# Performance work log

Measured on AMD Instinct MI355X. Metric: run time of the kernel, lower is better.

The kernel has to match this reference:

```python
import jax, jax.numpy as jnp
import numpy as np

B, S, HID = 2, 2048, 2048
H, D, KV = 16, 128, 4          # heads, head_dim, kv heads
REP = H // KV                  # GQA repeat factor
THETA = 10000.0


def setup_inputs() -> dict:
    key = jax.random.key(0)
    ks = jax.random.split(key, 12)
    query = jax.random.normal(ks[0], (B, S, HID), jnp.float32)
    k_in = jax.random.normal(ks[1], (B, S, HID), jnp.float32)
    v_in = jax.random.normal(ks[2], (B, S, HID), jnp.float32)
    # additive causal mask: 0 on/below diag, -10000 above
    causal = jnp.tril(jnp.ones((S, S), jnp.float32))
    mask = jnp.broadcast_to((1.0 - causal) * -10000.0, (B, 1, S, S))
    # rotary tables (cos/sin of freqs_cis), shape [S, D//2]
    inv_freq = 1.0 / (THETA ** (jnp.arange(0, D, 2, dtype=jnp.float32) / D))
    ang = jnp.outer(jnp.arange(S, dtype=jnp.float32), inv_freq)
    freqs_cos, freqs_sin = jnp.cos(ang), jnp.sin(ang)
    sd = 0.02
    Wq = jax.random.normal(ks[3], (HID, H * D), jnp.float32) * sd
    bq = jnp.zeros((H * D,), jnp.float32)
    Wk = jax.random.normal(ks[4], (HID, KV * D), jnp.float32) * sd
    bk = jnp.zeros((KV * D,), jnp.float32)
    Wv = jax.random.normal(ks[5], (HID, KV * D), jnp.float32) * sd
    bv = jnp.zeros((KV * D,), jnp.float32)
    Wo = jax.random.normal(ks[6], (H * D, HID), jnp.float32) * sd
    bo = jnp.zeros((HID,), jnp.float32)
    return {"query": query, "key": k_in, "value": v_in, "mask": mask,
            "freqs_cos": freqs_cos, "freqs_sin": freqs_sin,
            "Wq": Wq, "bq": bq, "Wk": Wk, "bk": bk,
            "Wv": Wv, "bv": bv, "Wo": Wo, "bo": bo}


def _rope(x, cos, sin):
    # x: [B,S,h,D]; pairs adjacent dims as complex (view_as_complex)
    xr = x.reshape(*x.shape[:-1], D // 2, 2)
    xe, xo = xr[..., 0], xr[..., 1]
    c = cos[None, :, None, :]
    s = sin[None, :, None, :]
    re = xe * c - xo * s
    im = xe * s + xo * c
    return jnp.stack([re, im], axis=-1).reshape(x.shape)


def reference(query, key, value, mask, freqs_cos, freqs_sin,
              Wq, bq, Wk, bk, Wv, bv, Wo, bo):
    q = (query @ Wq + bq).reshape(B, S, H, D)
    k = (key @ Wk + bk).reshape(B, S, KV, D)
    v = (value @ Wv + bv).reshape(B, S, KV, D)
    # repeat_kv: torch.repeat_interleave along head dim
    k = jnp.repeat(k, REP, axis=2)
    v = jnpp_repeat = jnp.repeat(v, REP, axis=2)
    q = _rope(q, freqs_cos, freqs_sin)
    k = _rope(k, freqs_cos, freqs_sin)
    q = q.transpose(0, 2, 1, 3)  # [B,H,S,D]
    k = k.transpose(0, 2, 1, 3)
    v = v.transpose(0, 2, 1, 3)
    scores = jnp.einsum('bhqd,bhkd->bhqk', q, k) / jnp.sqrt(jnp.float32(D))
    scores = scores + mask
    probs = jax.nn.softmax(scores, axis=-1)
    ctx = jnp.einsum('bhqk,bhkd->bhqd', probs, v)
    ctx = ctx.transpose(0, 2, 1, 3).reshape(B, S, H * D)
    return ctx @ Wo + bo
```

## Files before the change

kernel.cpp:

```cpp
#include <hip/hip_runtime.h>
#include <stdint.h>

#define BB 2
#define SS 2048
#define HID 2048
#define NH 16
#define DD 128
#define NKV 4

typedef unsigned short u16;
typedef __attribute__((ext_vector_type(8))) short short8;
typedef __attribute__((ext_vector_type(4))) float f32x4;

#if __has_builtin(__builtin_amdgcn_exp2f)
#define EXP2(x) __builtin_amdgcn_exp2f(x)
#else
#define EXP2(x) exp2f(x)
#endif

__device__ __forceinline__ u16 f2bf(float x) {
    union { float f; unsigned u; } v; v.f = x;
    unsigned u = v.u;
    return (u16)((u + 0x7FFFu + ((u >> 16) & 1u)) >> 16);
}

__device__ __forceinline__ void async_lds16(const void* g, void* l) {
    __builtin_amdgcn_global_load_lds(
        (const __attribute__((address_space(1))) void*)(uintptr_t)g,
        (__attribute__((address_space(3))) void*)(uintptr_t)l,
        16, 0, 0);
}

__global__ __launch_bounds__(256) void k_prep(const float* __restrict__ query,
                                              const float* __restrict__ key,
                                              const float* __restrict__ value,
                                              const float* __restrict__ Wq,
                                              const float* __restrict__ Wk,
                                              const float* __restrict__ Wv,
                                              const float* __restrict__ Wo,
                                              u16* __restrict__ qbf,
                                              u16* __restrict__ kbf,
                                              u16* __restrict__ vbf,
                                              u16* __restrict__ Wt,
                                              u16* __restrict__ Wot) {
    __shared__ float tile[32][33];
    int x = blockIdx.x;
    if (x < 24576) {
        const float* in; u16* out;
        if (x < 8192)       { in = query; out = qbf; }
        else if (x < 16384) { in = key;   out = kbf; x -= 8192; }
        else                { in = value; out = vbf; x -= 16384; }
        const int i = x * 256 + threadIdx.x;
        float4 v = ((const float4*)in)[i];
        uint2 o;
        o.x = (unsigned)f2bf(v.x) | ((unsigned)f2bf(v.y) << 16);
        o.y = (unsigned)f2bf(v.z) | ((unsigned)f2bf(v.w) << 16);
        ((uint2*)out)[i] = o;
        return;
    }
    const int v_ = x - 24576;
    const int ty = v_ / 160;
    const int xt = v_ - ty * 160;
    const float* src; u16* dst; int N, n0;
    if (xt < 64)      { src = Wq; dst = Wt;                          N = 2048; n0 = xt * 32; }
    else if (xt < 80) { src = Wk; dst = Wt + (size_t)2048 * 2048;    N = 512;  n0 = (xt - 64) * 32; }
    else if (xt < 96) { src = Wv; dst = Wt + (size_t)2560 * 2048;    N = 512;  n0 = (xt - 80) * 32; }
    else              { src = Wo; dst = Wot;                         N = 2048; n0 = (xt - 96) * 32; }
    const int k0 = ty * 32;
    const int c = threadIdx.x & 31, r = threadIdx.x >> 5;
#pragma unroll
    for (int i = 0; i < 32; i += 8)
        tile[r + i][c] = src[(size_t)(k0 + r + i) * N + n0 + c];
    __syncthreads();
#pragma unroll
    for (int i = 0; i < 32; i += 8)
        dst[(size_t)(n0 + r + i) * 2048 + k0 + c] = f2bf(tile[c][r + i]);
}

__global__ __launch_bounds__(256) void k_gemm_qkv(const u16* __restrict__ qbf,
                                                  const u16* __restrict__ kbf,
                                                  const u16* __restrict__ vbf,
                                                  const u16* __restrict__ Wt,
                                                  const float* __restrict__ bq,
                                                  const float* __restrict__ bk,
                                                  const float* __restrict__ bv,
                                                  const float* __restrict__ fc,
                                                  const float* __restrict__ fs,
                                                  u16* __restrict__ qro,
                                                  u16* __restrict__ kro,
                                                  u16* __restrict__ vtr) {
    __shared__ char smem[32768];
    u16* As = (u16*)smem;
    u16* Bs = (u16*)(smem + 16384);
    float* Ep = (float*)smem;

    const int tid = threadIdx.x;
    const int lane = tid & 63, wave = tid >> 6;
    const int bn = blockIdx.x;
    const int bm = blockIdx.y * 128;
    const u16* A = (bn < 16) ? qbf : (bn < 20) ? kbf : vbf;

    const int srow = wave * 8 + (lane >> 3);
    const int c0 = ((lane & 7) ^ (lane >> 3)) * 8;
    const u16* gA = A  + (size_t)(bm + srow) * 2048 + c0;
    const u16* gB = Wt + (size_t)(bn * 128 + srow) * 2048 + c0;

    const int r = lane & 15, q4 = lane >> 4;
    const int wm = (wave & 1) * 64, wn = (wave >> 1) * 64;

    int aoff[4][2], boff[4][2];
#pragma unroll
    for (int i = 0; i < 4; i++) {
        const int ar = wm + i * 16 + r;
        const int pa = q4 ^ (ar & 7);
        aoff[i][0] = ar * 64 + pa * 8;
        aoff[i][1] = ar * 64 + (pa ^ 4) * 8;
        const int br = wn + i * 16 + r;
        const int pb = q4 ^ (br & 7);
        boff[i][0] = br * 64 + pb * 8;
        boff[i][1] = br * 64 + (pb ^ 4) * 8;
    }

    f32x4 acc[4][4] = {};

    for (int kb = 0; kb < 2048; kb += 64) {
        async_lds16(gA,                       As + wave * 512);
        async_lds16(gA + (size_t)32 * 2048,   As + 2048 + wave * 512);
        async_lds16(gA + (size_t)64 * 2048,   As + 4096 + wave * 512);
        async_lds16(gA + (size_t)96 * 2048,   As + 6144 + wave * 512);
        async_lds16(gB,                       Bs + wave * 512);
        async_lds16(gB + (size_t)32 * 2048,   Bs + 2048 + wave * 512);
        async_lds16(gB + (size_t)64 * 2048,   Bs + 4096 + wave * 512);
        async_lds16(gB + (size_t)96 * 2048,   Bs + 6144 + wave * 512);
        gA += 64; gB += 64;
        __syncthreads();

#pragma unroll
        for (int kk = 0; kk < 2; kk++) {
            short8 av[4], bv_[4];
#pragma unroll
            for (int i = 0; i < 4; i++) av[i] = *(const short8*)(As + aoff[i][kk]);
#pragma unroll
            for (int j = 0; j < 4; j++) bv_[j] = *(const short8*)(Bs + boff[j][kk]);
#pragma unroll
            for (int i = 0; i < 4; i++)
#pragma unroll
                for (int j = 0; j < 4; j++)
                    acc[i][j] = __builtin_amdgcn_mfma_f32_16x16x32_bf16(av[i], bv_[j], acc[i][j], 0, 0, 0);
        }
        __syncthreads();
    }

    if (bn < 20) {
        const bool isQ = (bn < 16);
        const float qsc = isQ ? 0.08838834764831845f * 1.4426950408889634f : 1.0f;
        const float* bias = isQ ? bq : bk;
        const int head = isQ ? bn : (bn - 16);
        u16* base = isQ ? qro : kro;
        const int nheads = isQ ? NH : NKV;

        float* ep = Ep + wave * 1280;
        const int rowg = bm + wm + lane;
        const int s = rowg & 2047, bidx = rowg >> 11;
        const float* fcp0 = fc + s * 64;
        const float* fsp0 = fs + s * 64;

#pragma unroll
        for (int j = 0; j < 4; j++) {
            const float bcol = bias[head * 128 + wn + j * 16 + r];
#pragma unroll
            for (int i = 0; i < 4; i++)
#pragma unroll
                for (int g = 0; g < 4; g++)
                    ep[(i * 16 + q4 * 4 + g) * 20 + r] = acc[i][j][g] + bcol;
            float4 x0 = *(float4*)(ep + lane * 20 + 0);
            float4 x1 = *(float4*)(ep + lane * 20 + 4);
            float4 x2 = *(float4*)(ep + lane * 20 + 8);
            float4 x3 = *(float4*)(ep + lane * 20 + 12);
            const int d0 = wn + j * 16;
            const int ii0 = d0 >> 1;
            float4 ca = *(const float4*)(fcp0 + ii0);
            float4 cb = *(const float4*)(fcp0 + ii0 + 4);
            float4 sa = *(const float4*)(fsp0 + ii0);
            float4 sb = *(const float4*)(fsp0 + ii0 + 4);
            float o[16];
            o[0]  = (x0.x * ca.x - x0.y * sa.x) * qsc;  o[1]  = (x0.x * sa.x + x0.y * ca.x) * qsc;
            o[2]  = (x0.z * ca.y - x0.w * sa.y) * qsc;  o[3]  = (x0.z * sa.y + x0.w * ca.y) * qsc;
            o[4]  = (x1.x * ca.z - x1.y * sa.z) * qsc;  o[5]  = (x1.x * sa.z + x1.y * ca.z) * qsc;
            o[6]  = (x1.z * ca.w - x1.w * sa.w) * qsc;  o[7]  = (x1.z * sa.w + x1.w * ca.w) * qsc;
            o[8]  = (x2.x * cb.x - x2.y * sb.x) * qsc;  o[9]  = (x2.x * sb.x + x2.y * cb.x) * qsc;
            o[10] = (x2.z * cb.y - x2.w * sb.y) * qsc;  o[11] = (x2.z * sb.y + x2.w * cb.y) * qsc;
            o[12] = (x3.x * cb.z - x3.y * sb.z) * qsc;  o[13] = (x3.x * sb.z + x3.y * cb.z) * qsc;
            o[14] = (x3.z * cb.w - x3.w * sb.w) * qsc;  o[15] = (x3.z * sb.w + x3.w * cb.w) * qsc;
            unsigned w0 = (unsigned)f2bf(o[0])  | ((unsigned)f2bf(o[1])  << 16);
            unsigned w1 = (unsigned)f2bf(o[2])  | ((unsigned)f2bf(o[3])  << 16);
            unsigned w2 = (unsigned)f2bf(o[4])  | ((unsigned)f2bf(o[5])  << 16);
            unsigned w3 = (unsigned)f2bf(o[6])  | ((unsigned)f2bf(o[7])  << 16);
            unsigned w4 = (unsigned)f2bf(o[8])  | ((unsigned)f2bf(o[9])  << 16);
            unsigned w5 = (unsigned)f2bf(o[10]) | ((unsigned)f2bf(o[11]) << 16);
            unsigned w6 = (unsigned)f2bf(o[12]) | ((unsigned)f2bf(o[13]) << 16);
            unsigned w7 = (unsigned)f2bf(o[14]) | ((unsigned)f2bf(o[15]) << 16);
            u16* dst = base + (((size_t)(bidx * nheads + head) * SS + s) << 7) + d0;
            *(uint4*)dst = make_uint4(w0, w1, w2, w3);
            *(uint4*)(dst + 8) = make_uint4(w4, w5, w6, w7);
        }
    } else {
#pragma unroll
        for (int j = 0; j < 4; j++) {
            const int col = bn * 128 + wn + j * 16 + r - 2560;
            const int d = col & 127, kv = col >> 7;
            const float bb = bv[col];
#pragma unroll
            for (int i = 0; i < 4; i++) {
                const int row0 = bm + wm + i * 16 + q4 * 4;
                const int s0 = row0 & 2047, b = row0 >> 11;
                uint2 o;
                o.x = (unsigned)f2bf(acc[i][j][0] + bb) | ((unsigned)f2bf(acc[i][j][1] + bb) << 16);
                o.y = (unsigned)f2bf(acc[i][j][2] + bb) | ((unsigned)f2bf(acc[i][j][3] + bb) << 16);
                *(uint2*)(vtr + ((size_t)(b * NKV + kv) * DD + d) * SS + s0) = o;
            }
        }
    }
}

__global__ __launch_bounds__(256) void k_gemm_bt(const u16* __restrict__ A,
                                                 const u16* __restrict__ Bt,
                                                 const float* __restrict__ bias,
                                                 float* __restrict__ C,
                                                 int M, int N, int K) {
    __shared__ char smem[32768];
    u16* As = (u16*)smem;
    u16* Bs = (u16*)(smem + 16384);

    const int tid = threadIdx.x;
    const int lane = tid & 63, wave = tid >> 6;
    const int bm = blockIdx.y * 128, bn = blockIdx.x * 128;

    const int srow = wave * 8 + (lane >> 3);
    const int c0 = ((lane & 7) ^ (lane >> 3)) * 8;
    const u16* gA = A  + (size_t)(bm + srow) * K + c0;
    const u16* gB = Bt + (size_t)(bn + srow) * K + c0;

    const int r = lane & 15, q4 = lane >> 4;
    const int wm = (wave & 1) * 64, wn = (wave >> 1) * 64;

    int aoff[4][2], boff[4][2];
#pragma unroll
    for (int i = 0; i < 4; i++) {
        const int ar = wm + i * 16 + r;
        const int pa = q4 ^ (ar & 7);
        aoff[i][0] = ar * 64 + pa * 8;
        aoff[i][1] = ar * 64 + (pa ^ 4) * 8;
        const int br = wn + i * 16 + r;
        const int pb = q4 ^ (br & 7);
        boff[i][0] = br * 64 + pb * 8;
        boff[i][1] = br * 64 + (pb ^ 4) * 8;
    }

    f32x4 acc[4][4] = {};

    for (int kb = 0; kb < K; kb += 64) {
        async_lds16(gA,                    As + wave * 512);
        async_lds16(gA + (size_t)32 * K,   As + 2048 + wave * 512);
        async_lds16(gA + (size_t)64 * K,   As + 4096 + wave * 512);
        async_lds16(gA + (size_t)96 * K,   As + 6144 + wave * 512);
        async_lds16(gB,                    Bs + wave * 512);
        async_lds16(gB + (size_t)32 * K,   Bs + 2048 + wave * 512);
        async_lds16(gB + (size_t)64 * K,   Bs + 4096 + wave * 512);
        async_lds16(gB + (size_t)96 * K,   Bs + 6144 + wave * 512);
        gA += 64; gB += 64;
        __syncthreads();

#pragma unroll
        for (int kk = 0; kk < 2; kk++) {
            short8 av[4], bv_[4];
#pragma unroll
            for (int i = 0; i < 4; i++) av[i] = *(const short8*)(As + aoff[i][kk]);
#pragma unroll
            for (int j = 0; j < 4; j++) bv_[j] = *(const short8*)(Bs + boff[j][kk]);
#pragma unroll
            for (int i = 0; i < 4; i++)
#pragma unroll
                for (int j = 0; j < 4; j++)
                    acc[i][j] = __builtin_amdgcn_mfma_f32_16x16x32_bf16(av[i], bv_[j], acc[i][j], 0, 0, 0);
        }
        __syncthreads();
    }

#pragma unroll
    for (int j = 0; j < 4; j++) {
        const int col = bn + wn + j * 16 + r;
        const float bb = bias[col];
#pragma unroll
        for (int i = 0; i < 4; i++) {
            const int row = bm + wm + i * 16 + q4 * 4;
#pragma unroll
            for (int g = 0; g < 4; g++)
                C[(size_t)(row + g) * N + col] = acc[i][j][g] + bb;
        }
    }
}

__global__ __launch_bounds__(256) void k_attn(const u16* __restrict__ Q,
                                              const u16* __restrict__ K_,
                                              const u16* __restrict__ V_,
                                              u16* __restrict__ Ctx) {
    __shared__ u16 Ks[32 * 128];
    __shared__ u16 Vs[128 * 32];
    __shared__ u16 Pb[4 * 32 * 40];

    const int tid = threadIdx.x;
    const int lane = tid & 63, wave = tid >> 6;
    const int bh = blockIdx.x;
    const int b = bh >> 4, h = bh & 15;
    const int kvh = (b << 2) | (h >> 2);
    const int qb = (gridDim.y - 1 - blockIdx.y) * 128;
    const int qcol = lane & 15, q4 = lane >> 4;
    const int qw = qb + wave * 32;

    const u16* Qg = Q + ((size_t)bh * SS + qw + qcol) * DD;
    short8 qfr[2][4];
#pragma unroll
    for (int qi = 0; qi < 2; qi++)
#pragma unroll
        for (int c = 0; c < 4; c++)
            qfr[qi][c] = *(const short8*)(Qg + qi * 16 * DD + c * 32 + q4 * 8);

    const u16* Kg = K_ + (size_t)kvh * SS * DD;
    const u16* Vg = V_ + (size_t)kvh * DD * SS;

    const int krow = tid >> 4;
    const int kchunk = (tid & 15) ^ (krow & 7);
    const int vd = tid >> 2;
    const int vchunk = (tid & 3) ^ ((vd >> 1) & 3);

    f32x4 lacc[2] = {};
    f32x4 oacc[2][8] = {};

    const short8 ones = {0x3F80, 0x3F80, 0x3F80, 0x3F80, 0x3F80, 0x3F80, 0x3F80, 0x3F80};
    u16* pb = Pb + wave * 1280;
    unsigned* pb32 = (unsigned*)pb;

    for (int kb = 0; kb < qb + 128; kb += 32) {
        async_lds16(Kg + (size_t)(kb + krow) * DD + kchunk * 8,       Ks + wave * 512);
        async_lds16(Kg + (size_t)(kb + 16 + krow) * DD + kchunk * 8,  Ks + 2048 + wave * 512);
        async_lds16(Vg + (size_t)vd * SS + kb + vchunk * 8,           Vs + wave * 512);
        async_lds16(Vg + (size_t)(vd + 64) * SS + kb + vchunk * 8,    Vs + 2048 + wave * 512);
        __syncthreads();

        if (kb <= qw + 31) {
            f32x4 sc[2][2] = {};
#pragma unroll
            for (int kt = 0; kt < 2; kt++) {
                const int kr = kt * 16 + qcol;
#pragma unroll
                for (int c = 0; c < 4; c++) {
                    short8 kf = *(const short8*)(Ks + kr * 128 + (((c * 4 + q4) ^ (kr & 7)) << 3));
                    sc[kt][0] = __builtin_amdgcn_mfma_f32_16x16x32_bf16(kf, qfr[0][c], sc[kt][0], 0, 0, 0);
                    sc[kt][1] = __builtin_amdgcn_mfma_f32_16x16x32_bf16(kf, qfr[1][c], sc[kt][1], 0, 0, 0);
                }
            }

            if (kb + 32 > qw) {
#pragma unroll
                for (int kt = 0; kt < 2; kt++)
#pragma unroll
                    for (int qi = 0; qi < 2; qi++)
#pragma unroll
                        for (int g = 0; g < 4; g++) {
                            const int key = kb + kt * 16 + q4 * 4 + g;
                            if (key > qw + qi * 16 + qcol) sc[kt][qi][g] = -1e30f;
                        }
            }

            const unsigned sel = 0x07060302u;
#pragma unroll
            for (int qi = 0; qi < 2; qi++) {
                float p0 = EXP2(sc[0][qi][0]), p1 = EXP2(sc[0][qi][1]);
                float p2 = EXP2(sc[0][qi][2]), p3 = EXP2(sc[0][qi][3]);
                float p4 = EXP2(sc[1][qi][0]), p5 = EXP2(sc[1][qi][1]);
                float p6 = EXP2(sc[1][qi][2]), p7 = EXP2(sc[1][qi][3]);
                unsigned pk0 = __builtin_amdgcn_perm(__float_as_uint(p1), __float_as_uint(p0), sel);
                unsigned pk1 = __builtin_amdgcn_perm(__float_as_uint(p3), __float_as_uint(p2), sel);
                unsigned pk2 = __builtin_amdgcn_perm(__float_as_uint(p5), __float_as_uint(p4), sel);
                unsigned pk3 = __builtin_amdgcn_perm(__float_as_uint(p7), __float_as_uint(p6), sel);
                const int row = qi * 16 + qcol;
                *(uint2*)(pb32 + row * 20 + 2 * q4)     = make_uint2(pk0, pk1);
                *(uint2*)(pb32 + row * 20 + 8 + 2 * q4) = make_uint2(pk2, pk3);
            }

            short8 pf0 = *(const short8*)(pb + qcol * 40 + q4 * 8);
            short8 pf1 = *(const short8*)(pb + (16 + qcol) * 40 + q4 * 8);

            lacc[0] = __builtin_amdgcn_mfma_f32_16x16x32_bf16(ones, pf0, lacc[0], 0, 0, 0);
            lacc[1] = __builtin_amdgcn_mfma_f32_16x16x32_bf16(ones, pf1, lacc[1], 0, 0, 0);
#pragma unroll
            for (int dt = 0; dt < 8; dt++) {
                const int vr = dt * 16 + qcol;
                short8 vfr = *(const short8*)(Vs + vr * 32 + ((q4 ^ ((vr >> 1) & 3)) << 3));
                oacc[0][dt] = __builtin_amdgcn_mfma_f32_16x16x32_bf16(vfr, pf0, oacc[0][dt], 0, 0, 0);
                oacc[1][dt] = __builtin_amdgcn_mfma_f32_16x16x32_bf16(vfr, pf1, oacc[1][dt], 0, 0, 0);
            }
        }
        __syncthreads();
    }

#pragma unroll
    for (int qi = 0; qi < 2; qi++) {
        const float inv = 1.0f / lacc[qi][0];
        u16* outp = Ctx + ((size_t)b * SS + qw + qi * 16 + qcol) * (NH * DD) + h * DD;
#pragma unroll
        for (int dt = 0; dt < 8; dt++) {
            unsigned lo = (unsigned)f2bf(oacc[qi][dt][0] * inv) | ((unsigned)f2bf(oacc[qi][dt][1] * inv) << 16);
            unsigned hi = (unsigned)f2bf(oacc[qi][dt][2] * inv) | ((unsigned)f2bf(oacc[qi][dt][3] * inv) << 16);
            *(uint2*)(outp + dt * 16 + q4 * 4) = make_uint2(lo, hi);
        }
    }
}

extern "C" void kernel_launch(void* const* d_in, const int* in_sizes, int n_in,
                              void* d_out, int out_size, void* d_ws, size_t ws_size,
                              hipStream_t stream) {
    const float* query = (const float*)d_in[0];
    const float* key   = (const float*)d_in[1];
    const float* value = (const float*)d_in[2];
    const float* fc    = (const float*)d_in[4];
    const float* fs    = (const float*)d_in[5];
    const float* Wq    = (const float*)d_in[6];
    const float* bq    = (const float*)d_in[7];
    const float* Wk    = (const float*)d_in[8];
    const float* bk    = (const float*)d_in[9];
    const float* Wv    = (const float*)d_in[10];
    const float* bv    = (const float*)d_in[11];
    const float* Wo    = (const float*)d_in[12];
    const float* bo    = (const float*)d_in[13];
    float* out = (float*)d_out;

    char* w = (char*)d_ws;
    u16* qbf = (u16*)(w);
    u16* kbf = (u16*)(w + 16777216);
    u16* vbf = (u16*)(w + 33554432);
    u16* Wt  = (u16*)(w + 50331648);
    u16* Wot = (u16*)(w + 62914560);
    u16* qro = (u16*)(w + 71303168);
    u16* kro = (u16*)(w + 88080384);
    u16* vtr = (u16*)(w + 92274688);
    u16* ctx = (u16*)(w + 96468992);

    k_prep<<<34816, 256, 0, stream>>>(query, key, value, Wq, Wk, Wv, Wo,
                                      qbf, kbf, vbf, Wt, Wot);
    k_gemm_qkv<<<dim3(24, 32), 256, 0, stream>>>(qbf, kbf, vbf, Wt, bq, bk, bv,
                                                 fc, fs, qro, kro, vtr);
    k_attn<<<dim3(32, 16), 256, 0, stream>>>(qro, kro, vtr, ctx);
    k_gemm_bt<<<dim3(16, 32), 256, 0, stream>>>(ctx, Wot, bo, out, 4096, 2048, 2048);
}
```

Baseline: 400.5 us.

## Use 256x256 double-buffered pipelined GEMM tiles with 8 waves for projections

Replaces the 128x128 single-buffered GEMM loop in both the QKV projection and output projection with a shared 256x256-tile routine. It uses 512 threads, 128KB of LDS, double buffering, staggered async prefetch of A and B tiles interleaved with MFMA phases, and s_setprio around the compute. The goal is to hide global load latency and raise reuse per tile. The trade-off is far fewer blocks (192 and 128), which can under-fill the 256 CUs, plus heavy LDS use and register pressure.

```diff
diff --git a/kernel.cpp b/kernel.cpp
--- a/kernel.cpp
+++ b/kernel.cpp
@@ -77,142 +77,228 @@
         dst[(size_t)(n0 + r + i) * 2048 + k0 + c] = f2bf(tile[c][r + i]);
 }
 
-__global__ __launch_bounds__(256) void k_gemm_qkv(const u16* __restrict__ qbf,
-                                                  const u16* __restrict__ kbf,
-                                                  const u16* __restrict__ vbf,
-                                                  const u16* __restrict__ Wt,
-                                                  const float* __restrict__ bq,
-                                                  const float* __restrict__ bk,
-                                                  const float* __restrict__ bv,
-                                                  const float* __restrict__ fc,
-                                                  const float* __restrict__ fs,
-                                                  u16* __restrict__ qro,
-                                                  u16* __restrict__ kro,
-                                                  u16* __restrict__ vtr) {
-    __shared__ char smem[32768];
+__device__ __forceinline__ void gemm256_loop(const u16* __restrict__ gA,
+                                             const u16* __restrict__ gB,
+                                             const int K, char* smem,
+                                             const int wave, const int lane,
+                                             f32x4 (&acc)[8][4]) {
+    const int r = lane & 15, q4 = lane >> 4;
+    const int wr = wave >> 2, wc = wave & 3;
     u16* As = (u16*)smem;
-    u16* Bs = (u16*)(smem + 16384);
-    float* Ep = (float*)smem;
-
+    u16* Bs = (u16*)(smem + 65536);
+
+    int aoff[8], boff[4];
+#pragma unroll
+    for (int i = 0; i < 8; i++) {
+        const int ar = wr * 128 + i * 16 + r;
+        aoff[i] = ar * 64 + ((q4 ^ (ar & 7)) << 3);
+    }
+#pragma unroll
+    for (int j = 0; j < 4; j++) {
+        const int br = wc * 64 + j * 16 + r;
+        boff[j] = br * 64 + ((q4 ^ (br & 7)) << 3);
+    }
+
+    const int nt = K >> 6;
+
+#define STG_A(buf, i, T) async_lds16(gA + (size_t)(i) * 64 * K + (size_t)(T) * 64, \
+                                     smem + (buf) * 32768 + ((i) * 64 + wave * 8) * 128)
+#define STG_B(buf, i, T) async_lds16(gB + (size_t)(i) * 64 * K + (size_t)(T) * 64, \
+                                     smem + 65536 + (buf) * 32768 + ((i) * 64 + wave * 8) * 128)
+
+    STG_A(0, 0, 0); STG_A(0, 1, 0); STG_A(0, 2, 0); STG_A(0, 3, 0);
+    STG_B(0, 0, 0); STG_B(0, 1, 0); STG_B(0, 2, 0); STG_B(0, 3, 0);
+    STG_B(1, 0, 1); STG_B(1, 1, 1); STG_B(1, 2, 1); STG_B(1, 3, 1);
+    asm volatile("s_waitcnt vmcnt(4)" ::: "memory");
+    __builtin_amdgcn_s_barrier();
+
+    short8 Af[4][2], Bf[4][2];
+    for (int t = 0; t < nt; t++) {
+        const int cur = t & 1;
+        const u16* Ab = As + cur * 16384;
+        const u16* Bb = Bs + cur * 16384;
+        const bool p1v = (t + 1 < nt);
+        const bool p2v = (t + 2 < nt);
+
+#pragma unroll
+        for (int i = 0; i < 4; i++) {
+            Af[i][0] = *(const short8*)(Ab + aoff[i]);
+            Af[i][1] = *(const short8*)(Ab + (aoff[i] ^ 32));
+        }
+#pragma unroll
+        for (int j = 0; j < 2; j++) {
+            Bf[j][0] = *(const short8*)(Bb + boff[j]);
+            Bf[j][1] = *(const short8*)(Bb + (boff[j] ^ 32));
+        }
+        if (p1v) { STG_A(cur ^ 1, 0, t + 1); STG_A(cur ^ 1, 1, t + 1); }
+        __builtin_amdgcn_s_barrier();
+        asm volatile("s_waitcnt lgkmcnt(0)" ::: "memory");
+        __builtin_amdgcn_s_setprio(1);
+#pragma unroll
+        for (int kk = 0; kk < 2; kk++)
+#pragma unroll
+            for (int i = 0; i < 4; i++)
+#pragma unroll
+                for (int j = 0; j < 2; j++)
+                    acc[i][j] = __builtin_amdgcn_mfma_f32_16x16x32_bf16(Af[i][kk], Bf[j][kk], acc[i][j], 0, 0, 0);
+        __builtin_amdgcn_s_setprio(0);
+        __builtin_amdgcn_s_barrier();
+
+#pragma unroll
+        for (int j = 2; j < 4; j++) {
+            Bf[j][0] = *(const short8*)(Bb + boff[j]);
+            Bf[j][1] = *(const short8*)(Bb + (boff[j] ^ 32));
+        }
+        if (p1v) { STG_A(cur ^ 1, 2, t + 1); STG_A(cur ^ 1, 3, t + 1); }
+        __builtin_amdgcn_s_barrier();
+        asm volatile("s_waitcnt lgkmcnt(0)" ::: "memory");
+        __builtin_amdgcn_s_setprio(1);
+#pragma unroll
+        for (int kk = 0; kk < 2; kk++)
+#pragma unroll
+            for (int i = 0; i < 4; i++)
+#pragma unroll
+                for (int j = 2; j < 4; j++)
+                    acc[i][j] = __builtin_amdgcn_mfma_f32_16x16x32_bf16(Af[i][kk], Bf[j][kk], acc[i][j], 0, 0, 0);
+        __builtin_amdgcn_s_setprio(0);
+        __builtin_amdgcn_s_barrier();
+
+#pragma unroll
+        for (int i = 0; i < 4; i++) {
+            Af[i][0] = *(const short8*)(Ab + aoff[i + 4]);
+            Af[i][1] = *(const short8*)(Ab + (aoff[i + 4] ^ 32));
+        }
+        if (p2v) { STG_B(cur, 0, t + 2); STG_B(cur, 1, t + 2); }
+        __builtin_amdgcn_s_barrier();
+        asm volatile("s_waitcnt lgkmcnt(0)" ::: "memory");
+        __builtin_amdgcn_s_setprio(1);
+#pragma unroll
+        for (int kk = 0; kk < 2; kk++)
+#pragma unroll
+            for (int i = 0; i < 4; i++)
+#pragma unroll
+                for (int j = 2; j < 4; j++)
+                    acc[i + 4][j] = __builtin_amdgcn_mfma_f32_16x16x32_bf16(Af[i][kk], Bf[j][kk], acc[i + 4][j], 0, 0, 0);
+        __builtin_amdgcn_s_setprio(0);
+        __builtin_amdgcn_s_barrier();
+
+        if (p2v) {
+            STG_B(cur, 2, t + 2); STG_B(cur, 3, t + 2);
+            asm volatile("s_waitcnt vmcnt(4)" ::: "memory");
+        } else {
+            asm volatile("s_waitcnt vmcnt(0)" ::: "memory");
+        }
+        __builtin_amdgcn_s_barrier();
+        __builtin_amdgcn_s_setprio(1);
+#pragma unroll
+        for (int kk = 0; kk < 2; kk++)
+#pragma unroll
+            for (int i = 0; i < 4; i++)
+#pragma unroll
+                for (int j = 0; j < 2; j++)
+                    acc[i + 4][j] = __builtin_amdgcn_mfma_f32_16x16x32_bf16(Af[i][kk], Bf[j][kk], acc[i + 4][j], 0, 0, 0);
+        __builtin_amdgcn_s_setprio(0);
+        __builtin_amdgcn_s_barrier();
+    }
+#undef STG_A
+#undef STG_B
+}
+
+__global__ __launch_bounds__(512, 2) void k_gemm_qkv(const u16* __restrict__ qbf,
+                                                     const u16* __restrict__ kbf,
+                                                     const u16* __restrict__ vbf,
+                                                     const u16* __restrict__ Wt,
+                                                     const float* __restrict__ bq,
+                                                     const float* __restrict__ bk,
+                                                     const float* __restrict__ bv,
+                                                     const float* __restrict__ fc,
+                                                     const float* __restrict__ fs,
+                                                     u16* __restrict__ qro,
+                                                     u16* __restrict__ kro,
+                                                     u16* __restrict__ vtr) {
+    __shared__ char smem[131072];
     const int tid = threadIdx.x;
     const int lane = tid & 63, wave = tid >> 6;
-    const int bn = blockIdx.x;
-    const int bm = blockIdx.y * 128;
-    const u16* A = (bn < 16) ? qbf : (bn < 20) ? kbf : vbf;
+    const int wr = wave >> 2, wc = wave & 3;
+    const int r = lane & 15, q4 = lane >> 4;
+    const int bx = blockIdx.x;
+    const int bm0 = blockIdx.y * 256;
+    const u16* A = (bx < 8) ? qbf : (bx < 10) ? kbf : vbf;
 
     const int srow = wave * 8 + (lane >> 3);
     const int c0 = ((lane & 7) ^ (lane >> 3)) * 8;
-    const u16* gA = A  + (size_t)(bm + srow) * 2048 + c0;
-    const u16* gB = Wt + (size_t)(bn * 128 + srow) * 2048 + c0;
-
-    const int r = lane & 15, q4 = lane >> 4;
-    const int wm = (wave & 1) * 64, wn = (wave >> 1) * 64;
-
-    int aoff[4][2], boff[4][2];
-#pragma unroll
-    for (int i = 0; i < 4; i++) {
-        const int ar = wm + i * 16 + r;
-        const int pa = q4 ^ (ar & 7);
-        aoff[i][0] = ar * 64 + pa * 8;
-        aoff[i][1] = ar * 64 + (pa ^ 4) * 8;
-        const int br = wn + i * 16 + r;
-        const int pb = q4 ^ (br & 7);
-        boff[i][0] = br * 64 + pb * 8;
-        boff[i][1] = br * 64 + (pb ^ 4) * 8;
-    }
-
-    f32x4 acc[4][4] = {};
-
-    for (int kb = 0; kb < 2048; kb += 64) {
-        async_lds16(gA,                       As + wave * 512);
-        async_lds16(gA + (size_t)32 * 2048,   As + 2048 + wave * 512);
-        async_lds16(gA + (size_t)64 * 2048,   As + 4096 + wave * 512);
-        async_lds16(gA + (size_t)96 * 2048,   As + 6144 + wave * 512);
-        async_lds16(gB,                       Bs + wave * 512);
-        async_lds16(gB + (size_t)32 * 2048,   Bs + 2048 + wave * 512);
-        async_lds16(gB + (size_t)64 * 2048,   Bs + 4096 + wave * 512);
-        async_lds16(gB + (size_t)96 * 2048,   Bs + 6144 + wave * 512);
-        gA += 64; gB += 64;
-        __syncthreads();
-
-#pragma unroll
-        for (int kk = 0; kk < 2; kk++) {
-            short8 av[4], bv_[4];
-#pragma unroll
-            for (int i = 0; i < 4; i++) av[i] = *(const short8*)(As + aoff[i][kk]);
-#pragma unroll
-            for (int j = 0; j < 4; j++) bv_[j] = *(const short8*)(Bs + boff[j][kk]);
-#pragma unroll
-            for (int i = 0; i < 4; i++)
-#pragma unroll
-                for (int j = 0; j < 4; j++)
-                    acc[i][j] = __builtin_amdgcn_mfma_f32_16x16x32_bf16(av[i], bv_[j], acc[i][j], 0, 0, 0);
-        }
-        __syncthreads();
-    }
-
-    if (bn < 20) {
-        const bool isQ = (bn < 16);
+    const u16* gA = A  + (size_t)(bm0 + srow) * 2048 + c0;
+    const u16* gB = Wt + (size_t)(bx * 256 + srow) * 2048 + c0;
+
+    f32x4 acc[8][4] = {};
+    gemm256_loop(gA, gB, 2048, smem, wave, lane, acc);
+
+    if (bx < 10) {
+        const bool isQ = (bx < 8);
         const float qsc = isQ ? 0.08838834764831845f * 1.4426950408889634f : 1.0f;
         const float* bias = isQ ? bq : bk;
-        const int head = isQ ? bn : (bn - 16);
         u16* base = isQ ? qro : kro;
         const int nheads = isQ ? NH : NKV;
 
-        float* ep = Ep + wave * 1280;
-        const int rowg = bm + wm + lane;
-        const int s = rowg & 2047, bidx = rowg >> 11;
-        const float* fcp0 = fc + s * 64;
-        const float* fsp0 = fs + s * 64;
-
+        float* ep = (float*)smem + wave * 2560;
 #pragma unroll
         for (int j = 0; j < 4; j++) {
-            const float bcol = bias[head * 128 + wn + j * 16 + r];
-#pragma unroll
-            for (int i = 0; i < 4; i++)
+            const int gc = bx * 256 + wc * 64 + j * 16;
+            const int head = isQ ? (gc >> 7) : ((gc - 2048) >> 7);
+            const int d0 = gc & 127;
+            const float bcol = bias[head * 128 + d0 + r];
+#pragma unroll
+            for (int i = 0; i < 8; i++)
 #pragma unroll
                 for (int g = 0; g < 4; g++)
                     ep[(i * 16 + q4 * 4 + g) * 20 + r] = acc[i][j][g] + bcol;
-            float4 x0 = *(float4*)(ep + lane * 20 + 0);
-            float4 x1 = *(float4*)(ep + lane * 20 + 4);
-            float4 x2 = *(float4*)(ep + lane * 20 + 8);
-            float4 x3 = *(float4*)(ep + lane * 20 + 12);
-            const int d0 = wn + j * 16;
-            const int ii0 = d0 >> 1;
-            float4 ca = *(const float4*)(fcp0 + ii0);
-            float4 cb = *(const float4*)(fcp0 + ii0 + 4);
-            float4 sa = *(const float4*)(fsp0 + ii0);
-            float4 sb = *(const float4*)(fsp0 + ii0 + 4);
-            float o[16];
-            o[0]  = (x0.x * ca.x - x0.y * sa.x) * qsc;  o[1]  = (x0.x * sa.x + x0.y * ca.x) * qsc;
-            o[2]  = (x0.z * ca.y - x0.w * sa.y) * qsc;  o[3]  = (x0.z * sa.y + x0.w * ca.y) * qsc;
-            o[4]  = (x1.x * ca.z - x1.y * sa.z) * qsc;  o[5]  = (x1.x * sa.z + x1.y * ca.z) * qsc;
-            o[6]  = (x1.z * ca.w - x1.w * sa.w) * qsc;  o[7]  = (x1.z * sa.w + x1.w * ca.w) * qsc;
-            o[8]  = (x2.x * cb.x - x2.y * sb.x) * qsc;  o[9]  = (x2.x * sb.x + x2.y * cb.x) * qsc;
-            o[10] = (x2.z * cb.y - x2.w * sb.y) * qsc;  o[11] = (x2.z * sb.y + x2.w * cb.y) * qsc;
-            o[12] = (x3.x * cb.z - x3.y * sb.z) * qsc;  o[13] = (x3.x * sb.z + x3.y * cb.z) * qsc;
-            o[14] = (x3.z * cb.w - x3.w * sb.w) * qsc;  o[15] = (x3.z * sb.w + x3.w * cb.w) * qsc;
-            unsigned w0 = (unsigned)f2bf(o[0])  | ((unsigned)f2bf(o[1])  << 16);
-            unsigned w1 = (unsigned)f2bf(o[2])  | ((unsigned)f2bf(o[3])  << 16);
-            unsigned w2 = (unsigned)f2bf(o[4])  | ((unsigned)f2bf(o[5])  << 16);
-            unsigned w3 = (unsigned)f2bf(o[6])  | ((unsigned)f2bf(o[7])  << 16);
-            unsigned w4 = (unsigned)f2bf(o[8])  | ((unsigned)f2bf(o[9])  << 16);
-            unsigned w5 = (unsigned)f2bf(o[10]) | ((unsigned)f2bf(o[11]) << 16);
-            unsigned w6 = (unsigned)f2bf(o[12]) | ((unsigned)f2bf(o[13]) << 16);
-            unsigned w7 = (unsigned)f2bf(o[14]) | ((unsigned)f2bf(o[15]) << 16);
-            u16* dst = base + (((size_t)(bidx * nheads + head) * SS + s) << 7) + d0;
-            *(uint4*)dst = make_uint4(w0, w1, w2, w3);
-            *(uint4*)(dst + 8) = make_uint4(w4, w5, w6, w7);
+#pragma unroll
+            for (int rr = 0; rr < 2; rr++) {
+                const int row = rr * 64 + lane;
+                const int grow = bm0 + wr * 128 + row;
+                const int s = grow & 2047, bidx = grow >> 11;
+                const float* fcp0 = fc + s * 64;
+                const float* fsp0 = fs + s * 64;
+                float4 x0 = *(float4*)(ep + row * 20 + 0);
+                float4 x1 = *(float4*)(ep + row * 20 + 4);
+                float4 x2 = *(float4*)(ep + row * 20 + 8);
+                float4 x3 = *(float4*)(ep + row * 20 + 12);
+                const int ii0 = d0 >> 1;
+                float4 ca = *(const float4*)(fcp0 + ii0);
+                float4 cb = *(const float4*)(fcp0 + ii0 + 4);
+                float4 sa = *(const float4*)(fsp0 + ii0);
+                float4 sb = *(const float4*)(fsp0 + ii0 + 4);
+                float o[16];
+                o[0]  = (x0.x * ca.x - x0.y * sa.x) * qsc;  o[1]  = (x0.x * sa.x + x0.y * ca.x) * qsc;
+                o[2]  = (x0.z * ca.y - x0.w * sa.y) * qsc;  o[3]  = (x0.z * sa.y + x0.w * ca.y) * qsc;
+                o[4]  = (x1.x * ca.z - x1.y * sa.z) * qsc;  o[5]  = (x1.x * sa.z + x1.y * ca.z) * qsc;
+                o[6]  = (x1.z * ca.w - x1.w * sa.w) * qsc;  o[7]  = (x1.z * sa.w + x1.w * ca.w) * qsc;
+                o[8]  = (x2.x * cb.x - x2.y * sb.x) * qsc;  o[9]  = (x2.x * sb.x + x2.y * cb.x) * qsc;
+                o[10] = (x2.z * cb.y - x2.w * sb.y) * qsc;  o[11] = (x2.z * sb.y + x2.w * cb.y) * qsc;
+                o[12] = (x3.x * cb.z - x3.y * sb.z) * qsc;  o[13] = (x3.x * sb.z + x3.y * cb.z) * qsc;
+                o[14] = (x3.z * cb.w - x3.w * sb.w) * qsc;  o[15] = (x3.z * sb.w + x3.w * cb.w) * qsc;
+                unsigned w0 = (unsigned)f2bf(o[0])  | ((unsigned)f2bf(o[1])  << 16);
+                unsigned w1 = (unsigned)f2bf(o[2])  | ((unsigned)f2bf(o[3])  << 16);
+                unsigned w2 = (unsigned)f2bf(o[4])  | ((unsigned)f2bf(o[5])  << 16);
+                unsigned w3 = (unsigned)f2bf(o[6])  | ((unsigned)f2bf(o[7])  << 16);
+                unsigned w4 = (unsigned)f2bf(o[8])  | ((unsigned)f2bf(o[9])  << 16);
+                unsigned w5 = (unsigned)f2bf(o[10]) | ((unsigned)f2bf(o[11]) << 16);
+                unsigned w6 = (unsigned)f2bf(o[12]) | ((unsigned)f2bf(o[13]) << 16);
+                unsigned w7 = (unsigned)f2bf(o[14]) | ((unsigned)f2bf(o[15]) << 16);
+                u16* dst = base + (((size_t)(bidx * nheads + head) * SS + s) << 7) + d0;
+                *(uint4*)dst = make_uint4(w0, w1, w2, w3);
+                *(uint4*)(dst + 8) = make_uint4(w4, w5, w6, w7);
+            }
         }
     } else {
 #pragma unroll
         for (int j = 0; j < 4; j++) {
-            const int col = bn * 128 + wn + j * 16 + r - 2560;
-            const int d = col & 127, kv = col >> 7;
-            const float bb = bv[col];
-#pragma unroll
-            for (int i = 0; i < 4; i++) {
-                const int row0 = bm + wm + i * 16 + q4 * 4;
+            const int colb = bx * 256 + wc * 64 + j * 16 + r - 2560;
+            const int d = colb & 127, kv = colb >> 7;
+            const float bb = bv[colb];
+#pragma unroll
+            for (int i = 0; i < 8; i++) {
+                const int row0 = bm0 + wr * 128 + i * 16 + q4 * 4;
                 const int s0 = row0 & 2047, b = row0 >> 11;
                 uint2 o;
                 o.x = (unsigned)f2bf(acc[i][j][0] + bb) | ((unsigned)f2bf(acc[i][j][1] + bb) << 16);
@@ -223,77 +309,33 @@
     }
 }
 
-__global__ __launch_bounds__(256) void k_gemm_bt(const u16* __restrict__ A,
-                                                 const u16* __restrict__ Bt,
-                                                 const float* __restrict__ bias,
-                                                 float* __restrict__ C,
-                                                 int M, int N, int K) {
-    __shared__ char smem[32768];
-    u16* As = (u16*)smem;
-    u16* Bs = (u16*)(smem + 16384);
-
+__global__ __launch_bounds__(512, 2) void k_gemm_bt(const u16* __restrict__ A,
+                                                    const u16* __restrict__ Bt,
+                                                    const float* __restrict__ bias,
+                                                    float* __restrict__ C,
+                                                    int M, int N, int K) {
+    __shared__ char smem[131072];
     const int tid = threadIdx.x;
     const int lane = tid & 63, wave = tid >> 6;
-    const int bm = blockIdx.y * 128, bn = blockIdx.x * 128;
+    const int wr = wave >> 2, wc = wave & 3;
+    const int r = lane & 15, q4 = lane >> 4;
+    const int bm0 = blockIdx.y * 256, bn0 = blockIdx.x * 256;
 
     const int srow = wave * 8 + (lane >> 3);
     const int c0 = ((lane & 7) ^ (lane >> 3)) * 8;
-    const u16* gA = A  + (size_t)(bm + srow) * K + c0;
-    const u16* gB = Bt + (size_t)(bn + srow) * K + c0;
-
-    const int r = lane & 15, q4 = lane >> 4;
-    const int wm = (wave & 1) * 64, wn = (wave >> 1) * 64;
-
-    int aoff[4][2], boff[4][2];
-#pragma unroll
-    for (int i = 0; i < 4; i++) {
-        const int ar = wm + i * 16 + r;
-        const int pa = q4 ^ (ar & 7);
-        aoff[i][0] = ar * 64 + pa * 8;
-        aoff[i][1] = ar * 64 + (pa ^ 4) * 8;
-        const int br = wn + i * 16 + r;
-        const int pb = q4 ^ (br & 7);
-        boff[i][0] = br * 64 + pb * 8;
-        boff[i][1] = br * 64 + (pb ^ 4) * 8;
-    }
-
-    f32x4 acc[4][4] = {};
-
-    for (int kb = 0; kb < K; kb += 64) {
-        async_lds16(gA,                    As + wave * 512);
-        async_lds16(gA + (size_t)32 * K,   As + 2048 + wave * 512);
-        async_lds16(gA + (size_t)64 * K,   As + 4096 + wave * 512);
-        async_lds16(gA + (size_t)96 * K,   As + 6144 + wave * 512);
-        async_lds16(gB,                    Bs + wave * 512);
-        async_lds16(gB + (size_t)32 * K,   Bs + 2048 + wave * 512);
-        async_lds16(gB + (size_t)64 * K,   Bs + 4096 + wave * 512);
-        async_lds16(gB + (size_t)96 * K,   Bs + 6144 + wave * 512);
-        gA += 64; gB += 64;
-        __syncthreads();
-
-#pragma unroll
-        for (int kk = 0; kk < 2; kk++) {
-            short8 av[4], bv_[4];
-#pragma unroll
-            for (int i = 0; i < 4; i++) av[i] = *(const short8*)(As + aoff[i][kk]);
-#pragma unroll
-            for (int j = 0; j < 4; j++) bv_[j] = *(const short8*)(Bs + boff[j][kk]);
-#pragma unroll
-            for (int i = 0; i < 4; i++)
-#pragma unroll
-                for (int j = 0; j < 4; j++)
-                    acc[i][j] = __builtin_amdgcn_mfma_f32_16x16x32_bf16(av[i], bv_[j], acc[i][j], 0, 0, 0);
-        }
-        __syncthreads();
-    }
+    const u16* gA = A  + (size_t)(bm0 + srow) * K + c0;
+    const u16* gB = Bt + (size_t)(bn0 + srow) * K + c0;
+
+    f32x4 acc[8][4] = {};
+    gemm256_loop(gA, gB, K, smem, wave, lane, acc);
 
 #pragma unroll
     for (int j = 0; j < 4; j++) {
-        const int col = bn + wn + j * 16 + r;
+        const int col = bn0 + wc * 64 + j * 16 + r;
         const float bb = bias[col];
 #pragma unroll
-        for (int i = 0; i < 4; i++) {
-            const int row = bm + wm + i * 16 + q4 * 4;
+        for (int i = 0; i < 8; i++) {
+            const int row = bm0 + wr * 128 + i * 16 + q4 * 4;
 #pragma unroll
             for (int g = 0; g < 4; g++)
                 C[(size_t)(row + g) * N + col] = acc[i][j][g] + bb;
@@ -449,8 +491,8 @@
 
     k_prep<<<34816, 256, 0, stream>>>(query, key, value, Wq, Wk, Wv, Wo,
                                       qbf, kbf, vbf, Wt, Wot);
-    k_gemm_qkv<<<dim3(24, 32), 256, 0, stream>>>(qbf, kbf, vbf, Wt, bq, bk, bv,
+    k_gemm_qkv<<<dim3(12, 16), 512, 0, stream>>>(qbf, kbf, vbf, Wt, bq, bk, bv,
                                                  fc, fs, qro, kro, vtr);
     k_attn<<<dim3(32, 16), 256, 0, stream>>>(qro, kro, vtr, ctx);
-    k_gemm_bt<<<dim3(16, 32), 256, 0, stream>>>(ctx, Wot, bo, out, 4096, 2048, 2048);
-}
+    k_gemm_bt<<<dim3(8, 16), 512, 0, stream>>>(ctx, Wot, bo, out, 4096, 2048, 2048);
+}
```

Measured after the change: 405.4 us. Within noise of the previous version (+1.2%).
